# Performance work log

Hardware: AMD Instinct MI355X
Metric: run time of the kernel (lower is better)

## Reference

```python
import jax, jax.numpy as jnp
import numpy as np

N = 30000      # nodes
E = 300000     # directed edges (self loops added in conv)
G = 128        # graphs in the batch
IN = 128       # input_dim
HID = 64       # hidden per head
HEADS = 4
NC = 10        # num_classes
EPS = 1e-5
SLOPE = 0.2    # GATv2 leaky_relu negative slope


def setup_inputs() -> dict:
    key = jax.random.key(0)
    ks = jax.random.split(key, 40)
    d = {}
    d['x'] = jax.random.normal(ks[0], (N, IN), jnp.float32)
    d['edge_index'] = jax.random.randint(ks[1], (2, E), 0, N, jnp.int32)
    d['batch'] = jnp.sort(jax.random.randint(ks[2], (N,), 0, G, jnp.int32))
    in_ch = [IN, HID * HEADS, HID * HEADS, HID * HEADS]
    for i in range(4):
        oc = HID * HEADS if i < 3 else HID  # last layer concat=False -> HID
        sc = 1.0 / np.sqrt(in_ch[i])
        d[f'Wl{i}'] = jax.random.normal(ks[3 + 6 * i], (in_ch[i], HID * HEADS), jnp.float32) * sc
        d[f'Wr{i}'] = jax.random.normal(ks[4 + 6 * i], (in_ch[i], HID * HEADS), jnp.float32) * sc
        d[f'att{i}'] = jax.random.normal(ks[5 + 6 * i], (HEADS, HID), jnp.float32) * 0.1
        d[f'b{i}'] = jnp.zeros((oc,), jnp.float32)
        d[f'bng{i}'] = jnp.ones((oc,), jnp.float32)
        d[f'bnb{i}'] = jnp.zeros((oc,), jnp.float32)
    d['fc1_w'] = jax.random.normal(ks[30], (HID, HID), jnp.float32) / np.sqrt(HID)
    d['fc1_b'] = jnp.zeros((HID,), jnp.float32)
    d['fc2_w'] = jax.random.normal(ks[31], (HID, NC), jnp.float32) / np.sqrt(HID)
    d['fc2_b'] = jnp.zeros((NC,), jnp.float32)
    return d


def _gatv2_conv(h, src, dst, Wl, Wr, att, b, concat):
    # GATv2Conv: x_l = lin_l(x) for sources, x_r = lin_r(x) for targets
    xl = (h @ Wl).reshape(N, HEADS, HID)
    xr = (h @ Wr).reshape(N, HEADS, HID)
    z = jax.nn.leaky_relu(xl[src] + xr[dst], SLOPE)       # [Et, H, C]
    e = jnp.einsum('ehc,hc->eh', z, att)                   # [Et, H]
    m = jax.ops.segment_max(e, dst, num_segments=N)        # per-dst max
    p = jnp.exp(e - m[dst])
    s = jax.ops.segment_sum(p, dst, num_segments=N)
    alpha = p / s[dst]                                     # segment softmax
    msg = alpha[..., None] * xl[src]                       # [Et, H, C]
    out = jax.ops.segment_sum(msg, dst, num_segments=N)    # [N, H, C]
    out = out.reshape(N, HEADS * HID) if concat else out.mean(axis=1)
    return out + b


def _bn_train(h, g, b):
    mu = h.mean(axis=0)
    var = h.var(axis=0)  # biased, as torch BN uses for normalization
    return g * (h - mu) * jax.lax.rsqrt(var + EPS) + b


def _forward(x, edge_index, batch,
             Wl0, Wr0, att0, b0, bng0, bnb0,
             Wl1, Wr1, att1, b1, bng1, bnb1,
             Wl2, Wr2, att2, b2, bng2, bnb2,
             Wl3, Wr3, att3, b3, bng3, bnb3,
             fc1_w, fc1_b, fc2_w, fc2_b):
    loops = jnp.arange(N, dtype=edge_index.dtype)
    src = jnp.concatenate([edge_index[0], loops])  # add_self_loops=True
    dst = jnp.concatenate([edge_index[1], loops])
    layers = [(Wl0, Wr0, att0, b0, bng0, bnb0, True),
              (Wl1, Wr1, att1, b1, bng1, bnb1, True),
              (Wl2, Wr2, att2, b2, bng2, bnb2, True),
              (Wl3, Wr3, att3, b3, bng3, bnb3, False)]
    h = x
    for Wl, Wr, att, b, g, bb, concat in layers:
        h = jax.nn.elu(_bn_train(_gatv2_conv(h, src, dst, Wl, Wr, att, b, concat), g, bb))
    sums = jax.ops.segment_sum(h, batch, num_segments=G)
    cnt = jax.ops.segment_sum(jnp.ones((N,), h.dtype), batch, num_segments=G)
    pooled = sums / jnp.maximum(cnt, 1.0)[:, None]         # global_mean_pool
    o = jax.nn.relu(pooled @ fc1_w + fc1_b)
    return o @ fc2_w + fc2_b                               # dropout off (eval)


def reference(x, edge_index, batch,
              Wl0, Wr0, att0, b0, bng0, bnb0,
              Wl1, Wr1, att1, b1, bng1, bnb1,
              Wl2, Wr2, att2, b2, bng2, bnb2,
              Wl3, Wr3, att3, b3, bng3, bnb3,
              fc1_w, fc1_b, fc2_w, fc2_b):
    return _forward(x, edge_index, batch,
                    Wl0, Wr0, att0, b0, bng0, bnb0,
                    Wl1, Wr1, att1, b1, bng1, bnb1,
                    Wl2, Wr2, att2, b2, bng2, bnb2,
                    Wl3, Wr3, att3, b3, bng3, bnb3,
                    fc1_w, fc1_b, fc2_w, fc2_b)
```

## Files before the change

### kernel.cpp

```cpp
#include <hip/hip_runtime.h>
#include <hip/hip_bf16.h>
#include <math.h>

#define NN    30000
#define MPAD  30080
#define EE    300000
#define ETOT  330000
#define GG    128
#define IND   128
#define HIDD  64
#define NHEAD 4
#define CC    256
#define NCL   10
#define EPSBN 1e-5f
#define SLOPE 0.2f

typedef __attribute__((ext_vector_type(8))) __bf16 bf16x8;
typedef __attribute__((ext_vector_type(4))) float f32x4;
typedef __attribute__((ext_vector_type(2))) float f32x2;

__device__ inline float b2f(unsigned u16) {
    union { unsigned i; float f; } c; c.i = u16 << 16; return c.f;
}
__device__ inline unsigned short f2b(float f) {
    __hip_bfloat16 b = __float2bfloat16(f);
    unsigned short u; __builtin_memcpy(&u, &b, 2); return u;
}
__device__ inline f32x2 upk(unsigned u) {
    union { unsigned i; float f; } lo, hi;
    lo.i = u << 16;
    hi.i = u & 0xffff0000u;
    f32x2 r; r.x = lo.f; r.y = hi.f; return r;
}
__device__ inline void unpack8(uint4 u, float* f) {
    f[0] = b2f(u.x & 0xffffu); f[1] = b2f(u.x >> 16);
    f[2] = b2f(u.y & 0xffffu); f[3] = b2f(u.y >> 16);
    f[4] = b2f(u.z & 0xffffu); f[5] = b2f(u.z >> 16);
    f[6] = b2f(u.w & 0xffffu); f[7] = b2f(u.w >> 16);
}

struct WPtrs { const float* wl[4]; const float* wr[4]; };

__global__ void k_setup(const int* __restrict__ ei, int* __restrict__ deg,
                        WPtrs p, const float* __restrict__ x,
                        __hip_bfloat16* __restrict__ wt, __hip_bfloat16* __restrict__ hb) {
    int id = blockIdx.x * 256 + threadIdx.x;
    if (id < ETOT) {
        int d = (id < EE) ? ei[EE + id] : (id - EE);
        atomicAdd(&deg[d], 1);
        return;
    }
    int id1 = id - ETOT;
    if (id1 < 65536) {
        int n = id1 >> 7, k = id1 & 127;
        float v = (n < 256) ? p.wl[0][(size_t)k * 256 + n] : p.wr[0][(size_t)k * 256 + n - 256];
        wt[id1] = __float2bfloat16(v);
    } else if (id1 < 458752) {
        int id2 = id1 - 65536;
        int li = 1 + (id2 >> 17);
        int r = id2 & 131071;
        int n = r >> 8, k = r & 255;
        float v = (n < 256) ? p.wl[li][(size_t)k * 256 + n] : p.wr[li][(size_t)k * 256 + n - 256];
        wt[id1] = __float2bfloat16(v);
    } else {
        int id2 = id1 - 458752;
        if (id2 < NN * IND) hb[id2] = __float2bfloat16(x[id2]);
    }
}

__global__ void k_scan(const int* __restrict__ deg, int* __restrict__ rowptr,
                       int* __restrict__ cursor) {
    const int PER = 30;
    int t = threadIdx.x;
    int base = t * PER;
    int loc[PER];
    int s = 0;
    #pragma unroll
    for (int j = 0; j < PER; ++j) {
        int v = (base + j < NN) ? deg[base + j] : 0;
        loc[j] = s; s += v;
    }
    int lane = t & 63, wid = t >> 6;
    int v = s;
    #pragma unroll
    for (int d = 1; d < 64; d <<= 1) {
        int u = __shfl_up(v, d, 64);
        if (lane >= d) v += u;
    }
    __shared__ int wsum[16], woff[16];
    if (lane == 63) wsum[wid] = v;
    __syncthreads();
    if (t == 0) { int a = 0; for (int w2 = 0; w2 < 16; ++w2) { woff[w2] = a; a += wsum[w2]; } }
    __syncthreads();
    int excl = woff[wid] + (v - s);
    #pragma unroll
    for (int j = 0; j < PER; ++j) {
        int idx = base + j;
        if (idx <= NN) { int val = excl + loc[j]; rowptr[idx] = val; cursor[idx] = val; }
    }
}

__global__ void k_scatter(const int* __restrict__ ei, int* __restrict__ cursor,
                          int* __restrict__ csrc) {
    int e = blockIdx.x * blockDim.x + threadIdx.x;
    if (e >= ETOT) return;
    int s, d;
    if (e < EE) { s = ei[e]; d = ei[EE + e]; } else { s = e - EE; d = s; }
    int pos = atomicAdd(&cursor[d], 1);
    csrc[pos] = s;
}

template<int K>
__global__ __launch_bounds__(256) void k_gemm_mfma(
        const __hip_bfloat16* __restrict__ A, const __hip_bfloat16* __restrict__ Wt,
        __hip_bfloat16* __restrict__ xlb, __hip_bfloat16* __restrict__ xrb) {
    __shared__ __bf16 As[128 * 40];
    __shared__ __bf16 Bs[128 * 40];
    const int t = threadIdx.x;
    const int row0 = blockIdx.x * 128;
    const int col0 = blockIdx.y * 128;
    const int wv = t >> 6, lane = t & 63;
    const int wm = (wv & 1) * 64, wn = (wv >> 1) * 64;
    const int lm = lane & 15, lq = lane >> 4;
    const int sr0 = t >> 2, scc = (t & 3) * 8;
    const int sr1 = sr0 + 64;
    uint4 va0, va1, vb0, vb1;
    va0 = *(const uint4*)&A [(size_t)(row0 + sr0) * K + scc];
    va1 = *(const uint4*)&A [(size_t)(row0 + sr1) * K + scc];
    vb0 = *(const uint4*)&Wt[(size_t)(col0 + sr0) * K + scc];
    vb1 = *(const uint4*)&Wt[(size_t)(col0 + sr1) * K + scc];
    f32x4 acc[4][4] = {};
    for (int k0 = 0; k0 < K; k0 += 32) {
        *(uint4*)&As[sr0 * 40 + scc] = va0;
        *(uint4*)&As[sr1 * 40 + scc] = va1;
        *(uint4*)&Bs[sr0 * 40 + scc] = vb0;
        *(uint4*)&Bs[sr1 * 40 + scc] = vb1;
        __syncthreads();
        if (k0 + 32 < K) {
            int kn = k0 + 32;
            va0 = *(const uint4*)&A [(size_t)(row0 + sr0) * K + kn + scc];
            va1 = *(const uint4*)&A [(size_t)(row0 + sr1) * K + kn + scc];
            vb0 = *(const uint4*)&Wt[(size_t)(col0 + sr0) * K + kn + scc];
            vb1 = *(const uint4*)&Wt[(size_t)(col0 + sr1) * K + kn + scc];
        }
        bf16x8 af[4], bfr[4];
        #pragma unroll
        for (int i = 0; i < 4; ++i) {
            af[i]  = *(bf16x8*)&As[(wm + i * 16 + lm) * 40 + lq * 8];
            bfr[i] = *(bf16x8*)&Bs[(wn + i * 16 + lm) * 40 + lq * 8];
        }
        #pragma unroll
        for (int i = 0; i < 4; ++i)
            #pragma unroll
            for (int j = 0; j < 4; ++j)
                acc[i][j] = __builtin_amdgcn_mfma_f32_16x16x32_bf16(af[i], bfr[j], acc[i][j], 0, 0, 0);
        __syncthreads();
    }
    const int crow = lq * 4;
    __hip_bfloat16* O = (blockIdx.y < 2) ? xlb : xrb;
    const int cbase = (blockIdx.y & 1) * 128 + wn;
    #pragma unroll
    for (int j = 0; j < 4; ++j) {
        int oc = cbase + j * 16 + lm;
        #pragma unroll
        for (int i = 0; i < 4; ++i) {
            int grow = row0 + wm + i * 16 + crow;
            #pragma unroll
            for (int r = 0; r < 4; ++r)
                O[(size_t)(grow + r) * CC + oc] = __float2bfloat16(acc[i][j][r]);
        }
    }
}

template<bool CONCAT>
__global__ __launch_bounds__(256) void k_gat(const __hip_bfloat16* __restrict__ xlb,
        const __hip_bfloat16* __restrict__ xrb, const int* __restrict__ rowptr,
        const int* __restrict__ csrc, const float* __restrict__ att,
        __hip_bfloat16* __restrict__ outb, float* __restrict__ outf) {
    const int wv = threadIdx.x >> 6, lane = threadIdx.x & 63;
    const int n = blockIdx.x * 4 + wv;
    if (n >= NN) return;
    const int sub = lane >> 5, l5 = lane & 31;
    const float4* att4 = (const float4*)att;
    float4 a0 = att4[l5 * 2], a1 = att4[l5 * 2 + 1];
    f32x2 aw[4];
    aw[0].x = a0.x; aw[0].y = a0.y; aw[1].x = a0.z; aw[1].y = a0.w;
    aw[2].x = a1.x; aw[2].y = a1.y; aw[3].x = a1.z; aw[3].y = a1.w;
    const uint4* xl4 = (const uint4*)xlb;
    const uint4* xr4 = (const uint4*)xrb;
    uint4 xru = xr4[(size_t)n * 32 + l5];
    f32x2 xr2[4] = {upk(xru.x), upk(xru.y), upk(xru.z), upk(xru.w)};
    const int beg = rowptr[n], end = rowptr[n + 1];
    float ssum = 0.f;
    f32x2 acc[4] = {};
    const f32x2 slope2 = {SLOPE, SLOPE};
    for (int i0 = beg; i0 < end; i0 += 2) {
        int i = i0 + sub;
        bool valid = i < end;
        int s = csrc[valid ? i : end - 1];
        uint4 xu = xl4[(size_t)s * 32 + l5];
        f32x2 xl2[4] = {upk(xu.x), upk(xu.y), upk(xu.z), upk(xu.w)};
        f32x2 tv2 = {0.f, 0.f};
        #pragma unroll
        for (int j = 0; j < 4; ++j) {
            f32x2 v = xl2[j] + xr2[j];
            v = __builtin_elementwise_max(v, v * slope2);
            tv2 = __builtin_elementwise_fma(v, aw[j], tv2);
        }
        float tv = tv2.x + tv2.y;
        tv += __shfl_xor(tv, 1);
        tv += __shfl_xor(tv, 2);
        tv += __shfl_xor(tv, 4);
        float p = valid ? __expf(tv) : 0.f;
        ssum += p;
        f32x2 p2 = {p, p};
        #pragma unroll
        for (int j = 0; j < 4; ++j)
            acc[j] = __builtin_elementwise_fma(p2, xl2[j], acc[j]);
    }
    ssum += __shfl_xor(ssum, 32);
    float a[8] = {acc[0].x, acc[0].y, acc[1].x, acc[1].y,
                  acc[2].x, acc[2].y, acc[3].x, acc[3].y};
    #pragma unroll
    for (int j = 0; j < 8; ++j) a[j] += __shfl_xor(a[j], 32);
    float inv = 1.f / ssum;
    if (CONCAT) {
        if (sub == 0) {
            unsigned short r[8];
            #pragma unroll
            for (int j = 0; j < 8; ++j) r[j] = f2b(a[j] * inv);
            uint4 o;
            o.x = r[0] | ((unsigned)r[1] << 16); o.y = r[2] | ((unsigned)r[3] << 16);
            o.z = r[4] | ((unsigned)r[5] << 16); o.w = r[6] | ((unsigned)r[7] << 16);
            ((uint4*)outb)[(size_t)n * 32 + l5] = o;
        }
    } else {
        float v[8];
        #pragma unroll
        for (int j = 0; j < 8; ++j) {
            v[j] = a[j] * inv;
            v[j] += __shfl_xor(v[j], 8);
            v[j] += __shfl_xor(v[j], 16);
            v[j] *= 0.25f;
        }
        if (lane < 8) {
            ((float4*)outf)[(size_t)n * 16 + lane * 2]     = make_float4(v[0], v[1], v[2], v[3]);
            ((float4*)outf)[(size_t)n * 16 + lane * 2 + 1] = make_float4(v[4], v[5], v[6], v[7]);
        }
    }
}

__global__ __launch_bounds__(256) void k_bnstats256b(const __hip_bfloat16* __restrict__ in,
                                                     float* __restrict__ stats) {
    __shared__ float sh[512];
    int r0 = blockIdx.x * 128;
    int rend = min(r0 + 128, NN);
    int t = threadIdx.x;
    int half = t >> 7, tc = t & 127;
    float s0 = 0.f, s1 = 0.f, q0 = 0.f, q1 = 0.f;
    const unsigned* u32 = (const unsigned*)in;
    for (int r = r0 + half; r < rend; r += 2) {
        unsigned w = u32[(size_t)r * 128 + tc];
        float a = b2f(w & 0xffffu), b = b2f(w >> 16);
        s0 += a; q0 += a * a; s1 += b; q1 += b * b;
    }
    if (half) {
        sh[tc * 4 + 0] = s0; sh[tc * 4 + 1] = s1;
        sh[tc * 4 + 2] = q0; sh[tc * 4 + 3] = q1;
    }
    __syncthreads();
    if (!half) {
        s0 += sh[tc * 4 + 0]; s1 += sh[tc * 4 + 1];
        q0 += sh[tc * 4 + 2]; q1 += sh[tc * 4 + 3];
        atomicAdd(&stats[2 * tc], s0);       atomicAdd(&stats[2 * tc + 1], s1);
        atomicAdd(&stats[256 + 2 * tc], q0); atomicAdd(&stats[256 + 2 * tc + 1], q1);
    }
}

__global__ __launch_bounds__(256) void k_bnelu256b(const __hip_bfloat16* __restrict__ in,
        const float* __restrict__ stats, const float* __restrict__ gamma,
        const float* __restrict__ beta, __hip_bfloat16* __restrict__ outb) {
    int id = blockIdx.x * 256 + threadIdx.x;
    if (id >= NN * 32) return;
    int c0 = (id & 31) * 8;
    uint4 u = ((const uint4*)in)[id];
    float f[8]; unpack8(u, f);
    unsigned short r[8];
    #pragma unroll
    for (int j = 0; j < 8; ++j) {
        int c = c0 + j;
        float mu  = stats[c] * (1.f / NN);
        float var = stats[256 + c] * (1.f / NN) - mu * mu;
        float w = gamma[c] * rsqrtf(var + EPSBN);
        float v = w * (f[j] - mu) + beta[c];
        v = (v > 0.f) ? v : (__expf(v) - 1.f);
        r[j] = f2b(v);
    }
    uint4 o;
    o.x = r[0] | ((unsigned)r[1] << 16); o.y = r[2] | ((unsigned)r[3] << 16);
    o.z = r[4] | ((unsigned)r[5] << 16); o.w = r[6] | ((unsigned)r[7] << 16);
    ((uint4*)outb)[id] = o;
}

__global__ void k_bnstats64(const float* __restrict__ h, float* __restrict__ stats) {
    int r0 = blockIdx.x * 128;
    int rend = min(r0 + 128, NN);
    int c = threadIdx.x & 63;
    int ro = threadIdx.x >> 6;
    float s = 0.f, q = 0.f;
    for (int r = r0 + ro; r < rend; r += 4) {
        float v = h[(size_t)r * 64 + c];
        s += v; q += v * v;
    }
    atomicAdd(&stats[c], s); atomicAdd(&stats[64 + c], q);
}

__global__ void k_pool(const float* __restrict__ h, const int* __restrict__ batch,
                       const float* __restrict__ stats, const float* __restrict__ gamma,
                       const float* __restrict__ beta,
                       float* __restrict__ pooled, float* __restrict__ cnt) {
    int wv = threadIdx.x >> 6, lane = threadIdx.x & 63;
    int w = blockIdx.x * 4 + wv;
    int n0 = w * 64;
    if (n0 >= NN) return;
    int n1 = min(n0 + 64, NN);
    float mu  = stats[lane] * (1.f / NN);
    float var = stats[64 + lane] * (1.f / NN) - mu * mu;
    float sc = gamma[lane] * rsqrtf(var + EPSBN);
    float sh = beta[lane] - mu * sc;
    float sum = 0.f;
    int cur = batch[n0], c = 0;
    for (int n = n0; n < n1; ++n) {
        int g = batch[n];
        if (g != cur) {
            atomicAdd(&pooled[cur * 64 + lane], sum);
            if (lane == 0) atomicAdd(&cnt[cur], (float)c);
            sum = 0.f; c = 0; cur = g;
        }
        float v = fmaf(h[(size_t)n * 64 + lane], sc, sh);
        v = (v > 0.f) ? v : (__expf(v) - 1.f);
        sum += v;
        ++c;
    }
    atomicAdd(&pooled[cur * 64 + lane], sum);
    if (lane == 0) atomicAdd(&cnt[cur], (float)c);
}

__global__ void k_mlp(const float* __restrict__ pooled, const float* __restrict__ cnt,
        const float* __restrict__ w1, const float* __restrict__ b1,
        const float* __restrict__ w2, const float* __restrict__ b2,
        float* __restrict__ out) {
    __shared__ float p[64], o[64];
    int g = blockIdx.x, t = threadIdx.x;
    float c = fmaxf(cnt[g], 1.f);
    p[t] = pooled[g * 64 + t] / c;
    __syncthreads();
    float s = b1[t];
    for (int k = 0; k < 64; ++k) s += p[k] * w1[k * 64 + t];
    o[t] = fmaxf(s, 0.f);
    __syncthreads();
    if (t < NCL) {
        float s2 = b2[t];
        for (int k = 0; k < 64; ++k) s2 += o[k] * w2[k * NCL + t];
        out[g * NCL + t] = s2;
    }
}

extern "C" void kernel_launch(void* const* d_in, const int* in_sizes, int n_in,
                              void* d_out, int out_size, void* d_ws, size_t ws_size,
                              hipStream_t stream) {
    const float* x     = (const float*)d_in[0];
    const int*   ei    = (const int*)d_in[1];
    const int*   batch = (const int*)d_in[2];
    WPtrs wp;
    const float *attp[4], *bng[4], *bnb[4];
    for (int i = 0; i < 4; ++i) {
        wp.wl[i] = (const float*)d_in[3 + 6 * i];
        wp.wr[i] = (const float*)d_in[4 + 6 * i];
        attp[i]  = (const float*)d_in[5 + 6 * i];
        bng[i]   = (const float*)d_in[7 + 6 * i];
        bnb[i]   = (const float*)d_in[8 + 6 * i];
    }
    const float* fc1w = (const float*)d_in[27];
    const float* fc1b = (const float*)d_in[28];
    const float* fc2w = (const float*)d_in[29];
    const float* fc2b = (const float*)d_in[30];
    float* out = (float*)d_out;

    char* w = (char*)d_ws;
    __hip_bfloat16* xlb  = (__hip_bfloat16*)w; w += (size_t)MPAD * CC * 2;
    __hip_bfloat16* xrb  = (__hip_bfloat16*)w; w += (size_t)MPAD * CC * 2;
    __hip_bfloat16* bufB = (__hip_bfloat16*)w; w += (size_t)MPAD * CC * 2;
    __hip_bfloat16* hb   = (__hip_bfloat16*)w; w += (size_t)MPAD * CC * 2;
    __hip_bfloat16* wt   = (__hip_bfloat16*)w; w += (size_t)458752 * 2;
    float* bufF   = (float*)w; w += (size_t)NN * HIDD * 4;
    int*   rowptr = (int*)w;   w += (size_t)(NN + 1) * 4;
    int*   cursor = (int*)w;   w += (size_t)(NN + 1) * 4;
    int*   csrc   = (int*)w;   w += (size_t)ETOT * 4;
    char* zbase = w;
    int*   deg       = (int*)w;   w += (size_t)NN * 4;
    float* stats_all = (float*)w; w += (size_t)4 * 512 * 4;
    float* pooled    = (float*)w; w += (size_t)GG * HIDD * 4;
    float* cnt       = (float*)w; w += (size_t)GG * 4;
    size_t zbytes = (size_t)(w - zbase);

    __hip_bfloat16* Wt[4];
    Wt[0] = wt;
    Wt[1] = wt + 65536;
    Wt[2] = wt + 65536 + 131072;
    Wt[3] = wt + 65536 + 262144;

    hipMemsetAsync(zbase, 0, zbytes, stream);
    k_setup<<<(ETOT + 458752 + NN * IND + 255) / 256, 256, 0, stream>>>(ei, deg, wp, x, wt, hb);
    k_scan<<<1, 1024, 0, stream>>>(deg, rowptr, cursor);
    k_scatter<<<(ETOT + 255) / 256, 256, 0, stream>>>(ei, cursor, csrc);

    for (int L = 0; L < 4; ++L) {
        float* stats = stats_all + 512 * L;
        dim3 gg(MPAD / 128, 4);
        if (L == 0) k_gemm_mfma<IND><<<gg, 256, 0, stream>>>(hb, Wt[0], xlb, xrb);
        else        k_gemm_mfma<CC><<<gg, 256, 0, stream>>>(hb, Wt[L], xlb, xrb);
        if (L < 3) {
            k_gat<true><<<NN / 4, 256, 0, stream>>>(xlb, xrb, rowptr, csrc, attp[L], bufB, nullptr);
            k_bnstats256b<<<(NN + 127) / 128, 256, 0, stream>>>(bufB, stats);
            k_bnelu256b<<<(NN * 32 + 255) / 256, 256, 0, stream>>>(bufB, stats, bng[L], bnb[L], hb);
        } else {
            k_gat<false><<<NN / 4, 256, 0, stream>>>(xlb, xrb, rowptr, csrc, attp[3], nullptr, bufF);
            k_bnstats64<<<(NN + 127) / 128, 256, 0, stream>>>(bufF, stats);
        }
    }
    k_pool<<<((NN + 63) / 64 + 3) / 4, 256, 0, stream>>>(bufF, batch, stats_all + 512 * 3,
                                                         bng[3], bnb[3], pooled, cnt);
    k_mlp<<<GG, 64, 0, stream>>>(pooled, cnt, fc1w, fc1b, fc2w, fc2b, out);
}
```

Baseline: 594.2 us.

## Fuse BN+ELU into GEMM A-load and finalize BN stats in last block

Removes the separate BN+ELU kernel for hidden layers: the stats kernel now has its last block, chosen through an atomic counter, compute per-channel scale and shift. The next layer's GEMM applies the affine transform and ELU while staging A tiles into shared memory. The GEMM epilogue is also changed to go through shared memory so that each row is written with coalesced 16-byte stores. This saves a full read and write of the activation per layer, but each GEMM column block now recomputes ELU on its A tiles, adding exp work inside the GEMM mainloop.

```diff
diff --git a/kernel.cpp b/kernel.cpp
--- a/kernel.cpp
+++ b/kernel.cpp
@@ -110,12 +110,14 @@
     csrc[pos] = s;
 }
 
-template<int K>
+template<int K, bool FUSE>
 __global__ __launch_bounds__(256) void k_gemm_mfma(
         const __hip_bfloat16* __restrict__ A, const __hip_bfloat16* __restrict__ Wt,
+        const float2* __restrict__ scsh,
         __hip_bfloat16* __restrict__ xlb, __hip_bfloat16* __restrict__ xrb) {
-    __shared__ __bf16 As[128 * 40];
-    __shared__ __bf16 Bs[128 * 40];
+    __shared__ __align__(16) char smem[20480];
+    __bf16* As = (__bf16*)smem;
+    __bf16* Bs = As + 128 * 40;
     const int t = threadIdx.x;
     const int row0 = blockIdx.x * 128;
     const int col0 = blockIdx.y * 128;
@@ -131,8 +133,30 @@
     vb1 = *(const uint4*)&Wt[(size_t)(col0 + sr1) * K + scc];
     f32x4 acc[4][4] = {};
     for (int k0 = 0; k0 < K; k0 += 32) {
-        *(uint4*)&As[sr0 * 40 + scc] = va0;
-        *(uint4*)&As[sr1 * 40 + scc] = va1;
+        if (FUSE) {
+            float f0[8], f1[8];
+            unpack8(va0, f0); unpack8(va1, f1);
+            unsigned short r0[8], r1[8];
+            #pragma unroll
+            for (int j = 0; j < 8; ++j) {
+                float2 ss = scsh[k0 + scc + j];
+                float v0 = fmaf(f0[j], ss.x, ss.y);
+                float v1 = fmaf(f1[j], ss.x, ss.y);
+                v0 = (v0 > 0.f) ? v0 : (__expf(v0) - 1.f);
+                v1 = (v1 > 0.f) ? v1 : (__expf(v1) - 1.f);
+                r0[j] = f2b(v0); r1[j] = f2b(v1);
+            }
+            uint4 w0, w1;
+            w0.x = r0[0] | ((unsigned)r0[1] << 16); w0.y = r0[2] | ((unsigned)r0[3] << 16);
+            w0.z = r0[4] | ((unsigned)r0[5] << 16); w0.w = r0[6] | ((unsigned)r0[7] << 16);
+            w1.x = r1[0] | ((unsigned)r1[1] << 16); w1.y = r1[2] | ((unsigned)r1[3] << 16);
+            w1.z = r1[4] | ((unsigned)r1[5] << 16); w1.w = r1[6] | ((unsigned)r1[7] << 16);
+            *(uint4*)&As[sr0 * 40 + scc] = w0;
+            *(uint4*)&As[sr1 * 40 + scc] = w1;
+        } else {
+            *(uint4*)&As[sr0 * 40 + scc] = va0;
+            *(uint4*)&As[sr1 * 40 + scc] = va1;
+        }
         *(uint4*)&Bs[sr0 * 40 + scc] = vb0;
         *(uint4*)&Bs[sr1 * 40 + scc] = vb1;
         __syncthreads();
@@ -156,19 +180,26 @@
                 acc[i][j] = __builtin_amdgcn_mfma_f32_16x16x32_bf16(af[i], bfr[j], acc[i][j], 0, 0, 0);
         __syncthreads();
     }
-    const int crow = lq * 4;
     __hip_bfloat16* O = (blockIdx.y < 2) ? xlb : xrb;
     const int cbase = (blockIdx.y & 1) * 128 + wn;
+    unsigned short* tb = (unsigned short*)smem + wv * (32 * 72);
     #pragma unroll
-    for (int j = 0; j < 4; ++j) {
-        int oc = cbase + j * 16 + lm;
-        #pragma unroll
-        for (int i = 0; i < 4; ++i) {
-            int grow = row0 + wm + i * 16 + crow;
+    for (int p = 0; p < 2; ++p) {
+        #pragma unroll
+        for (int ii = 0; ii < 2; ++ii) {
+            int i = p * 2 + ii;
             #pragma unroll
-            for (int r = 0; r < 4; ++r)
-                O[(size_t)(grow + r) * CC + oc] = __float2bfloat16(acc[i][j][r]);
-        }
+            for (int j = 0; j < 4; ++j)
+                #pragma unroll
+                for (int r = 0; r < 4; ++r)
+                    tb[(ii * 16 + lq * 4 + r) * 72 + j * 16 + lm] = f2b(acc[i][j][r]);
+        }
+        int lr = lane >> 1, h = lane & 1;
+        const uint4* src = (const uint4*)&tb[lr * 72 + h * 32];
+        uint4 q0 = src[0], q1 = src[1], q2 = src[2], q3 = src[3];
+        int grow = row0 + wm + p * 32 + lr;
+        uint4* dst = (uint4*)&O[(size_t)grow * CC + cbase + h * 32];
+        dst[0] = q0; dst[1] = q1; dst[2] = q2; dst[3] = q3;
     }
 }
 
@@ -251,8 +282,11 @@
 }
 
 __global__ __launch_bounds__(256) void k_bnstats256b(const __hip_bfloat16* __restrict__ in,
-                                                     float* __restrict__ stats) {
+        float* __restrict__ stats, const float* __restrict__ gamma,
+        const float* __restrict__ beta, float2* __restrict__ scsh,
+        int* __restrict__ counter) {
     __shared__ float sh[512];
+    __shared__ int lastf;
     int r0 = blockIdx.x * 128;
     int rend = min(r0 + 128, NN);
     int t = threadIdx.x;
@@ -275,31 +309,21 @@
         atomicAdd(&stats[2 * tc], s0);       atomicAdd(&stats[2 * tc + 1], s1);
         atomicAdd(&stats[256 + 2 * tc], q0); atomicAdd(&stats[256 + 2 * tc + 1], q1);
     }
-}
-
-__global__ __launch_bounds__(256) void k_bnelu256b(const __hip_bfloat16* __restrict__ in,
-        const float* __restrict__ stats, const float* __restrict__ gamma,
-        const float* __restrict__ beta, __hip_bfloat16* __restrict__ outb) {
-    int id = blockIdx.x * 256 + threadIdx.x;
-    if (id >= NN * 32) return;
-    int c0 = (id & 31) * 8;
-    uint4 u = ((const uint4*)in)[id];
-    float f[8]; unpack8(u, f);
-    unsigned short r[8];
-    #pragma unroll
-    for (int j = 0; j < 8; ++j) {
-        int c = c0 + j;
-        float mu  = stats[c] * (1.f / NN);
+    __syncthreads();
+    if (t == 0) {
+        __threadfence();
+        int old = atomicAdd(counter, 1);
+        lastf = (old == (int)gridDim.x - 1);
+    }
+    __syncthreads();
+    if (lastf) {
+        __threadfence();
+        int c = t;
+        float mu = stats[c] * (1.f / NN);
         float var = stats[256 + c] * (1.f / NN) - mu * mu;
         float w = gamma[c] * rsqrtf(var + EPSBN);
-        float v = w * (f[j] - mu) + beta[c];
-        v = (v > 0.f) ? v : (__expf(v) - 1.f);
-        r[j] = f2b(v);
-    }
-    uint4 o;
-    o.x = r[0] | ((unsigned)r[1] << 16); o.y = r[2] | ((unsigned)r[3] << 16);
-    o.z = r[4] | ((unsigned)r[5] << 16); o.w = r[6] | ((unsigned)r[7] << 16);
-    ((uint4*)outb)[id] = o;
+        scsh[c] = make_float2(w, beta[c] - mu * w);
+    }
 }
 
 __global__ void k_bnstats64(const float* __restrict__ h, float* __restrict__ stats) {
@@ -391,17 +415,19 @@
     __hip_bfloat16* xlb  = (__hip_bfloat16*)w; w += (size_t)MPAD * CC * 2;
     __hip_bfloat16* xrb  = (__hip_bfloat16*)w; w += (size_t)MPAD * CC * 2;
     __hip_bfloat16* bufB = (__hip_bfloat16*)w; w += (size_t)MPAD * CC * 2;
-    __hip_bfloat16* hb   = (__hip_bfloat16*)w; w += (size_t)MPAD * CC * 2;
+    __hip_bfloat16* hb   = (__hip_bfloat16*)w; w += (size_t)MPAD * IND * 2;
     __hip_bfloat16* wt   = (__hip_bfloat16*)w; w += (size_t)458752 * 2;
-    float* bufF   = (float*)w; w += (size_t)NN * HIDD * 4;
-    int*   rowptr = (int*)w;   w += (size_t)(NN + 1) * 4;
-    int*   cursor = (int*)w;   w += (size_t)(NN + 1) * 4;
-    int*   csrc   = (int*)w;   w += (size_t)ETOT * 4;
+    float*  bufF   = (float*)w;  w += (size_t)NN * HIDD * 4;
+    float2* scsh   = (float2*)w; w += (size_t)3 * 256 * 8;
+    int*    rowptr = (int*)w;    w += (size_t)(NN + 1) * 4;
+    int*    cursor = (int*)w;    w += (size_t)(NN + 1) * 4;
+    int*    csrc   = (int*)w;    w += (size_t)ETOT * 4;
     char* zbase = w;
     int*   deg       = (int*)w;   w += (size_t)NN * 4;
     float* stats_all = (float*)w; w += (size_t)4 * 512 * 4;
     float* pooled    = (float*)w; w += (size_t)GG * HIDD * 4;
     float* cnt       = (float*)w; w += (size_t)GG * 4;
+    int*   bncnt     = (int*)w;   w += (size_t)4 * 4;
     size_t zbytes = (size_t)(w - zbase);
 
     __hip_bfloat16* Wt[4];
@@ -418,12 +444,14 @@
     for (int L = 0; L < 4; ++L) {
         float* stats = stats_all + 512 * L;
         dim3 gg(MPAD / 128, 4);
-        if (L == 0) k_gemm_mfma<IND><<<gg, 256, 0, stream>>>(hb, Wt[0], xlb, xrb);
-        else        k_gemm_mfma<CC><<<gg, 256, 0, stream>>>(hb, Wt[L], xlb, xrb);
+        if (L == 0)
+            k_gemm_mfma<IND, false><<<gg, 256, 0, stream>>>(hb, Wt[0], nullptr, xlb, xrb);
+        else
+            k_gemm_mfma<CC, true><<<gg, 256, 0, stream>>>(bufB, Wt[L], scsh + (L - 1) * 256, xlb, xrb);
         if (L < 3) {
             k_gat<true><<<NN / 4, 256, 0, stream>>>(xlb, xrb, rowptr, csrc, attp[L], bufB, nullptr);
-            k_bnstats256b<<<(NN + 127) / 128, 256, 0, stream>>>(bufB, stats);
-            k_bnelu256b<<<(NN * 32 + 255) / 256, 256, 0, stream>>>(bufB, stats, bng[L], bnb[L], hb);
+            k_bnstats256b<<<(NN + 127) / 128, 256, 0, stream>>>(bufB, stats, bng[L], bnb[L],
+                                                                scsh + L * 256, bncnt + L);
         } else {
             k_gat<false><<<NN / 4, 256, 0, stream>>>(xlb, xrb, rowptr, csrc, attp[3], nullptr, bufF);
             k_bnstats64<<<(NN + 127) / 128, 256, 0, stream>>>(bufF, stats);
```

New measurement: 608.2 us. +2.4%, slower.
